# Kernel tuning notes

Measured on AMD Instinct MI355X. Metric: run time of the kernel, lower is better.

## Reference

```python
import jax, jax.numpy as jnp
import numpy as np

B, L, D, NH, K, R = 2, 1024, 768, 12, 24, 768
HD = D // NH            # head_dim = 64
NFFT = 2048             # nearest power of two >= 2*L-1


def _spectral_filters():
    # Hankel matrix Z_{ij} = 2 / ((i+j)^3 - (i+j)), top-K eigvecs scaled by sigma^{1/4}
    e = np.arange(1, L + 1, dtype=np.float64)
    ipj = e[:, None] + e[None, :]
    Z = 2.0 / (ipj ** 3 - ipj)
    sigma, phi = np.linalg.eigh(Z)
    phi_k = phi[:, -K:] * (sigma[-K:] ** 0.25)
    return jnp.asarray(phi_k, dtype=jnp.float32)  # (L, K)


def setup_inputs() -> dict:
    key = jax.random.key(0)
    ks = jax.random.split(key, 16)
    s = 0.02
    lin = lambda k_, i, o: jax.random.normal(k_, (i, o), jnp.float32) * s
    return {
        "x": jax.random.normal(ks[0], (B, L, D), jnp.float32),
        "stu_filters": _spectral_filters(),
        "M_inputs": jax.random.normal(ks[1], (D, R), jnp.float32) * s,
        "M_filters": jax.random.normal(ks[2], (K, R), jnp.float32) * s,
        "wq_w": lin(ks[3], D, D), "wq_b": jnp.zeros((D,), jnp.float32),
        "wk_w": lin(ks[4], D, D), "wk_b": jnp.zeros((D,), jnp.float32),
        "wv_w": lin(ks[5], D, D), "wv_b": jnp.zeros((D,), jnp.float32),
        "wg_w": lin(ks[6], D, D), "wg_b": jnp.zeros((D,), jnp.float32),
        "wo_w": lin(ks[7], D, D), "wo_b": jnp.zeros((D,), jnp.float32),
    }


def _stu_features(x, stu_filters, M_inputs, M_filters):
    # tensordot STU path: project inputs and filters to rank R, then FFT causal conv
    u = x @ M_inputs                       # (B, L, R)
    phi = stu_filters @ M_filters          # (L, R)
    sgn = jnp.where(jnp.arange(L) % 2 == 0, 1.0, -1.0)[None, :, None]  # (1, L, 1)
    V = jnp.fft.rfft(phi, n=NFFT, axis=0)  # (NFFT//2+1, R)
    U = jnp.stack([u, u * sgn], axis=-1)   # (B, L, R, 2)
    Uf = jnp.fft.rfft(U, n=NFFT, axis=1)   # (B, NFFT//2+1, R, 2)
    conv = jnp.fft.irfft(V[None, :, :, None] * Uf, n=NFFT, axis=1)[:, :L]  # (B, L, R, 2)
    u_plus = conv[..., 0]
    u_minus = conv[..., 1] * sgn
    return u_plus + u_minus               # (B, L, R) with R == D


def reference(x, stu_filters, M_inputs, M_filters,
              wq_w, wq_b, wk_w, wk_b, wv_w, wv_b,
              wg_w, wg_b, wo_w, wo_b):
    x_tilde = _stu_features(x, stu_filters, M_inputs, M_filters)  # (B, L, D)

    heads = lambda y: y.reshape(B, L, NH, HD).transpose(0, 2, 1, 3)  # (B, H, L, h)
    q = heads(x @ wq_w + wq_b)
    k = heads(x @ wk_w + wk_b)
    v = heads(x @ wv_w + wv_b)

    # causal linear attention via cumulative outer-product state
    Z = jnp.einsum('bhtp,bhtn->bhtpn', v, k)     # (B, H, L, h, h)
    Hc = jnp.cumsum(Z, axis=2)
    Y = jnp.einsum('bhtp,bhtpn->bhtn', q, Hc)    # (B, H, L, h)
    y_attn = Y.transpose(0, 2, 1, 3).reshape(B, L, D)

    gate = jax.nn.sigmoid(x @ wg_w + wg_b)
    y = x_tilde + (y_attn - x_tilde) * gate
    return y @ wo_w + wo_b
```

## Files before the change

kernel.cpp:

```cpp
#include <hip/hip_runtime.h>
#include <math.h>

#define B_  2
#define L_  1024
#define D_  768
#define NH_ 12
#define HD_ 64
#define K_  24
#define R_  768
#define NC_ 16
#define CS_ 64

typedef __bf16 bf16x8 __attribute__((ext_vector_type(8)));
typedef float f32x4 __attribute__((ext_vector_type(4)));
typedef float f32x8 __attribute__((ext_vector_type(8)));
typedef unsigned short u16x8 __attribute__((ext_vector_type(8)));

__device__ inline unsigned short f2bf(float f) {
    union { float f; unsigned u; } v; v.f = f;
    unsigned r = v.u + 0x7FFFu + ((v.u >> 16) & 1u);
    return (unsigned short)(r >> 16);
}

__device__ inline ushort4 pack4(const f32x4 v) {
    ushort4 r;
    r.x = f2bf(v[0]); r.y = f2bf(v[1]); r.z = f2bf(v[2]); r.w = f2bf(v[3]);
    return r;
}

__device__ inline u16x8 pack8(const f32x8 v) {
    u16x8 r;
#pragma unroll
    for (int e = 0; e < 8; ++e) r[e] = f2bf(v[e]);
    return r;
}

__device__ inline f32x8 bf2f8(const u16x8 v) {
    f32x8 r;
#pragma unroll
    for (int e = 0; e < 8; ++e) {
        union { float f; unsigned u; } t;
        t.u = ((unsigned)v[e]) << 16;
        r[e] = t.f;
    }
    return r;
}

#define GLD_LDS16(g, l)                                                     \
    __builtin_amdgcn_global_load_lds(                                       \
        (const __attribute__((address_space(1))) void*)(g),                 \
        (__attribute__((address_space(3))) void*)(l), 16, 0, 0)

__global__ __launch_bounds__(256) void k_prep(const float* __restrict__ w0,
                                              const float* __restrict__ w1,
                                              const float* __restrict__ w2,
                                              const float* __restrict__ w3,
                                              const float* __restrict__ w4,
                                              const float* __restrict__ w5,
                                              unsigned short* __restrict__ Wt,
                                              const float* __restrict__ x,
                                              unsigned short* __restrict__ xb) {
    const int bid = blockIdx.x;
    const int tid = threadIdx.x;
    if (bid < 864) {
        const int z = bid / 144, rem = bid % 144;
        const float* W;
        switch (z) {
            case 0: W = w0; break;
            case 1: W = w1; break;
            case 2: W = w2; break;
            case 3: W = w3; break;
            case 4: W = w4; break;
            default: W = w5; break;
        }
        unsigned short* o = Wt + (size_t)z * D_ * D_;
        __shared__ float t[64][69];
        const int n0 = (rem % 12) * 64, k0 = (rem / 12) * 64;
        const int row = tid >> 4, c4 = (tid & 15) * 4;
#pragma unroll
        for (int i = 0; i < 4; ++i) {
            const float4 v = *reinterpret_cast<const float4*>(
                W + (size_t)(k0 + row + i * 16) * D_ + n0 + c4);
            t[row + i * 16][c4 + 0] = v.x;
            t[row + i * 16][c4 + 1] = v.y;
            t[row + i * 16][c4 + 2] = v.z;
            t[row + i * 16][c4 + 3] = v.w;
        }
        __syncthreads();
        const int orow = tid >> 4, oc4 = (tid & 15) * 4;
#pragma unroll
        for (int i = 0; i < 4; ++i) {
            const int nn = orow + i * 16;
            ushort4 o4;
            o4.x = f2bf(t[oc4 + 0][nn]);
            o4.y = f2bf(t[oc4 + 1][nn]);
            o4.z = f2bf(t[oc4 + 2][nn]);
            o4.w = f2bf(t[oc4 + 3][nn]);
            *reinterpret_cast<ushort4*>(o + (size_t)(n0 + nn) * D_ + k0 + oc4) = o4;
        }
    } else {
        const int i8 = ((bid - 864) * 256 + tid) * 8;
        float4 f0 = *reinterpret_cast<const float4*>(x + i8);
        float4 f1 = *reinterpret_cast<const float4*>(x + i8 + 4);
        u16x8 p;
        p[0] = f2bf(f0.x); p[1] = f2bf(f0.y); p[2] = f2bf(f0.z); p[3] = f2bf(f0.w);
        p[4] = f2bf(f1.x); p[5] = f2bf(f1.y); p[6] = f2bf(f1.z); p[7] = f2bf(f1.w);
        *reinterpret_cast<u16x8*>(xb + i8) = p;
    }
}

template <int FM, int FN>
__device__ __forceinline__ void gemm_core(const unsigned short* __restrict__ A,
                                          const unsigned short* __restrict__ Bt,
                                          const float* __restrict__ bias,
                                          int mode,
                                          float* __restrict__ cf,
                                          unsigned short* __restrict__ cbf,
                                          unsigned short* __restrict__ ct,
                                          int N, int Kd,
                                          int bm, int bn, int tid) {
    constexpr int BM = 2 * FM * 16;
    constexpr int BN = 2 * FN * 16;
    constexpr int CTS = BM + 4;
    __shared__ unsigned short smem[2 * BM * 64 + 2 * BN * 64];
    unsigned short (*As)[BM * 64] = (unsigned short (*)[BM * 64])smem;
    unsigned short (*Bs)[BN * 64] = (unsigned short (*)[BN * 64])(smem + 2 * BM * 64);
    const int lane = tid & 63, wave = tid >> 6;
    const int wm = (wave >> 1) * (FM * 16), wn = (wave & 1) * (FN * 16);
    const int l15 = lane & 15, lg = lane >> 4;

    f32x4 acc[FM][FN] = {};

    auto stage = [&](int buf, int k0) {
#pragma unroll
        for (int q = 0; q < FM; ++q) {
            const int s = q * 256 + tid;
            GLD_LDS16(A + (size_t)(bm + (s >> 3)) * Kd + k0 + (s & 7) * 8,
                      &As[buf][s * 8]);
        }
#pragma unroll
        for (int q = 0; q < FN; ++q) {
            const int s = q * 256 + tid;
            GLD_LDS16(Bt + (size_t)(bn + (s >> 3)) * Kd + k0 + (s & 7) * 8,
                      &Bs[buf][s * 8]);
        }
    };

    stage(0, 0);
    __syncthreads();
    int cur = 0;
    const int nt = Kd / 64;
    for (int t = 0; t < nt; ++t) {
        if (t + 1 < nt) stage(cur ^ 1, (t + 1) * 64);
#pragma unroll
        for (int ks = 0; ks < 2; ++ks) {
            const int kb = ks * 32 + lg * 8;
            bf16x8 a[FM], b[FN];
#pragma unroll
            for (int f = 0; f < FM; ++f)
                a[f] = *reinterpret_cast<const bf16x8*>(
                    &As[cur][(wm + f * 16 + l15) * 64 + kb]);
#pragma unroll
            for (int f = 0; f < FN; ++f)
                b[f] = *reinterpret_cast<const bf16x8*>(
                    &Bs[cur][(wn + f * 16 + l15) * 64 + kb]);
#pragma unroll
            for (int fm = 0; fm < FM; ++fm)
#pragma unroll
                for (int fn = 0; fn < FN; ++fn)
                    acc[fm][fn] = __builtin_amdgcn_mfma_f32_16x16x32_bf16(
                        a[fm], b[fn], acc[fm][fn], 0, 0, 0);
        }
        __syncthreads();
        cur ^= 1;
    }

#pragma unroll
    for (int fm = 0; fm < FM; ++fm)
#pragma unroll
        for (int fn = 0; fn < FN; ++fn) {
            const int cl = wn + fn * 16 + l15;
            const int col = bn + cl;
            const float bv = bias ? bias[col] : 0.f;
            const int rl = wm + fm * 16 + lg * 4;
            const int r0 = bm + rl;
            f32x4 v = acc[fm][fn];
            v[0] += bv; v[1] += bv; v[2] += bv; v[3] += bv;
            if (mode == 0) {
#pragma unroll
                for (int j = 0; j < 4; ++j)
                    cf[(size_t)(r0 + j) * N + col] = v[j];
            }
            if (mode & 1) {
#pragma unroll
                for (int j = 0; j < 4; ++j)
                    cbf[(size_t)(r0 + j) * D_ + col] = f2bf(v[j]);
            }
            if (mode & 2) {
                *reinterpret_cast<ushort4*>(&smem[cl * CTS + rl]) = pack4(v);
            }
        }

    if (mode & 2) {
        __syncthreads();
        const int bI = bm >> 10, l0 = bm & 1023;
#pragma unroll
        for (int q = 0; q < BN * BM / 8 / 256; ++q) {
            const int slot = q * 256 + tid;
            const int cl = slot / (BM / 8), seg = slot % (BM / 8);
            const int gcol = bn + cl;
            const int h = gcol >> 6, n = gcol & 63;
            *reinterpret_cast<u16x8*>(
                ct + (((size_t)bI * NH_ + h) * 64 + n) * (size_t)L_ + l0 + seg * 8) =
                *reinterpret_cast<const u16x8*>(&smem[cl * CTS + seg * 8]);
        }
    }
}

__global__ __launch_bounds__(256) void k_gemm(const unsigned short* __restrict__ A,
                                              const unsigned short* __restrict__ Bt,
                                              const float* __restrict__ bias,
                                              float* __restrict__ C,
                                              int N, int Kd) {
    gemm_core<1, 2>(A, Bt, bias, 0, C, nullptr, nullptr, N, Kd,
                    blockIdx.y * 32, blockIdx.x * 64, threadIdx.x);
}

__global__ __launch_bounds__(256) void k_gemm5(const unsigned short* __restrict__ A,
                                               const unsigned short* __restrict__ wt,
                                               const float* __restrict__ bq,
                                               const float* __restrict__ bk,
                                               const float* __restrict__ bv,
                                               const float* __restrict__ bg,
                                               unsigned short* __restrict__ ubf,
                                               unsigned short* __restrict__ qbf,
                                               unsigned short* __restrict__ ktb,
                                               unsigned short* __restrict__ vbf,
                                               unsigned short* __restrict__ vtb,
                                               unsigned short* __restrict__ gbf) {
    const int z = blockIdx.z;
    const float* bias = nullptr;
    int mode = 1;
    unsigned short* cbf = nullptr; unsigned short* ct = nullptr;
    switch (z) {
        case 0: mode = 1; cbf = ubf; bias = nullptr; break;
        case 1: mode = 1; cbf = qbf; bias = bq; break;
        case 2: mode = 2; ct = ktb; bias = bk; break;
        case 3: mode = 3; cbf = vbf; ct = vtb; bias = bv; break;
        default: mode = 1; cbf = gbf; bias = bg; break;
    }
    const unsigned short* Bt = wt + (size_t)z * D_ * D_;
    gemm_core<4, 4>(A, Bt, bias, mode, nullptr, cbf, ct, D_, D_,
                    blockIdx.y * 128, blockIdx.x * 128, threadIdx.x);
}

__global__ __launch_bounds__(256) void k_attn(const unsigned short* __restrict__ qbf,
                                              const unsigned short* __restrict__ vbf,
                                              const unsigned short* __restrict__ ktb,
                                              const unsigned short* __restrict__ vtb,
                                              unsigned short* __restrict__ yab,
                                              const float* __restrict__ F,
                                              const float* __restrict__ Mf,
                                              unsigned short* __restrict__ phiev) {
    const int tid = threadIdx.x;
    if (blockIdx.x >= 384) {
        const int idx = ((int)blockIdx.x - 384) * 256 + tid;
        const int r = idx % R_;
        const int n = idx / R_;
        float acc = 0.f;
#pragma unroll
        for (int kk = 0; kk < K_; ++kk)
            acc += F[(2 * n) * K_ + kk] * Mf[kk * R_ + r];
        phiev[idx] = f2bf(2.f * acc);
        return;
    }
    const int c = blockIdx.x & 15, h = (blockIdx.x >> 4) % NH_, b = blockIdx.x / (16 * NH_);
    __shared__ unsigned short Qs[64 * 64];
    __shared__ unsigned short Vs[64 * 64];
    __shared__ unsigned short Kc[64 * 64];
    __shared__ unsigned short Tk[2][64 * 64];
    __shared__ unsigned short Tv[2][64 * 64];
    __shared__ unsigned short Sl[64 * 72];
    __shared__ unsigned short Hl[64 * 72];

    const int lane = tid & 63, wave = tid >> 6;
    const int wr = (wave >> 1) * 32, wc = (wave & 1) * 32;
    const int l15 = lane & 15, lg = lane >> 4;

    {
        const size_t rowbase = ((size_t)(b * L_ + c * CS_)) * D_ + h * HD_;
        const size_t tbase = ((size_t)(b * NH_ + h)) * 64 * (size_t)L_ + c * 64;
#pragma unroll
        for (int q2 = 0; q2 < 2; ++q2) {
            const int s = q2 * 256 + tid;
            const int row = s >> 3, c8 = s & 7;
            GLD_LDS16(qbf + rowbase + (size_t)row * D_ + c8 * 8, &Qs[s * 8]);
            GLD_LDS16(vbf + rowbase + (size_t)row * D_ + c8 * 8, &Vs[s * 8]);
            GLD_LDS16(ktb + tbase + (size_t)row * L_ + c8 * 8, &Kc[s * 8]);
        }
    }

    auto stage_t = [&](int buf, int cc) {
        const size_t tb2 = ((size_t)(b * NH_ + h)) * 64 * (size_t)L_ + cc * 64;
#pragma unroll
        for (int q2 = 0; q2 < 2; ++q2) {
            const int s = q2 * 256 + tid;
            const int row = s >> 3, c8 = s & 7;
            GLD_LDS16(ktb + tb2 + (size_t)row * L_ + c8 * 8, &Tk[buf][s * 8]);
            GLD_LDS16(vtb + tb2 + (size_t)row * L_ + c8 * 8, &Tv[buf][s * 8]);
        }
    };

    if (c > 0) stage_t(0, 0);
    __syncthreads();

    f32x4 hacc[2][2] = {};
    int cur = 0;
    for (int cc = 0; cc < c; ++cc) {
        if (cc + 1 < c) stage_t(cur ^ 1, cc + 1);
#pragma unroll
        for (int ks = 0; ks < 2; ++ks) {
            const int kb = ks * 32 + lg * 8;
            bf16x8 av[2], bk[2];
#pragma unroll
            for (int f = 0; f < 2; ++f) {
                av[f] = *reinterpret_cast<const bf16x8*>(&Tv[cur][(wr + f * 16 + l15) * 64 + kb]);
                bk[f] = *reinterpret_cast<const bf16x8*>(&Tk[cur][(wc + f * 16 + l15) * 64 + kb]);
            }
#pragma unroll
            for (int fm = 0; fm < 2; ++fm)
#pragma unroll
                for (int fn = 0; fn < 2; ++fn)
                    hacc[fm][fn] = __builtin_amdgcn_mfma_f32_16x16x32_bf16(
                        av[fm], bk[fn], hacc[fm][fn], 0, 0, 0);
        }
        __syncthreads();
        cur ^= 1;
    }

    if (c > 0) {
#pragma unroll
        for (int fm = 0; fm < 2; ++fm)
#pragma unroll
            for (int fn = 0; fn < 2; ++fn) {
                const int n = wc + fn * 16 + l15;
                const int p0 = wr + fm * 16 + lg * 4;
                *reinterpret_cast<ushort4*>(&Hl[n * 72 + p0]) = pack4(hacc[fm][fn]);
            }
    }

    {
        f32x4 sacc[2][2] = {};
#pragma unroll
        for (int ks = 0; ks < 2; ++ks) {
            const int kb = ks * 32 + lg * 8;
            bf16x8 av[2], bq[2];
#pragma unroll
            for (int f = 0; f < 2; ++f) {
                av[f] = *reinterpret_cast<const bf16x8*>(&Vs[(wr + f * 16 + l15) * 64 + kb]);
                bq[f] = *reinterpret_cast<const bf16x8*>(&Qs[(wc + f * 16 + l15) * 64 + kb]);
            }
#pragma unroll
            for (int fm = 0; fm < 2; ++fm)
#pragma unroll
                for (int fn = 0; fn < 2; ++fn)
                    sacc[fm][fn] = __builtin_amdgcn_mfma_f32_16x16x32_bf16(
                        av[fm], bq[fn], sacc[fm][fn], 0, 0, 0);
        }
#pragma unroll
        for (int fm = 0; fm < 2; ++fm)
#pragma unroll
            for (int fn = 0; fn < 2; ++fn) {
                const int t = wc + fn * 16 + l15;
                const int s0 = wr + fm * 16 + lg * 4;
#pragma unroll
                for (int j = 0; j < 4; ++j)
                    if (s0 + j > t) sacc[fm][fn][j] = 0.f;
                *reinterpret_cast<ushort4*>(&Sl[t * 72 + s0]) = pack4(sacc[fm][fn]);
            }
    }
    __syncthreads();

    f32x4 yacc[2][2] = {};
#pragma unroll
    for (int ks = 0; ks < 2; ++ks) {
        const int kb = ks * 32 + lg * 8;
        bf16x8 ak[2], bs[2];
#pragma unroll
        for (int f = 0; f < 2; ++f) {
            ak[f] = *reinterpret_cast<const bf16x8*>(&Kc[(wr + f * 16 + l15) * 64 + kb]);
            bs[f] = *reinterpret_cast<const bf16x8*>(&Sl[(wc + f * 16 + l15) * 72 + kb]);
        }
#pragma unroll
        for (int fm = 0; fm < 2; ++fm)
#pragma unroll
            for (int fn = 0; fn < 2; ++fn)
                yacc[fm][fn] = __builtin_amdgcn_mfma_f32_16x16x32_bf16(
                    ak[fm], bs[fn], yacc[fm][fn], 0, 0, 0);
    }
    if (c > 0) {
#pragma unroll
        for (int ks = 0; ks < 2; ++ks) {
            const int kb = ks * 32 + lg * 8;
            bf16x8 ah[2], bq[2];
#pragma unroll
            for (int f = 0; f < 2; ++f) {
                ah[f] = *reinterpret_cast<const bf16x8*>(&Hl[(wr + f * 16 + l15) * 72 + kb]);
                bq[f] = *reinterpret_cast<const bf16x8*>(&Qs[(wc + f * 16 + l15) * 64 + kb]);
            }
#pragma unroll
            for (int fm = 0; fm < 2; ++fm)
#pragma unroll
                for (int fn = 0; fn < 2; ++fn)
                    yacc[fm][fn] = __builtin_amdgcn_mfma_f32_16x16x32_bf16(
                        ah[fm], bq[fn], yacc[fm][fn], 0, 0, 0);
        }
    }

#pragma unroll
    for (int fm = 0; fm < 2; ++fm)
#pragma unroll
        for (int fn = 0; fn < 2; ++fn) {
            const int n0 = wr + fm * 16 + lg * 4;
            const int t = wc + fn * 16 + l15;
            const size_t idx = ((size_t)(b * L_ + c * CS_ + t)) * D_ + h * HD_ + n0;
            *reinterpret_cast<ushort4*>(yab + idx) = pack4(yacc[fm][fn]);
        }
}

__global__ __launch_bounds__(768) void k_conv(const unsigned short* __restrict__ ubf,
                                              const unsigned short* __restrict__ phiev,
                                              const unsigned short* __restrict__ yab,
                                              const unsigned short* __restrict__ gbf,
                                              unsigned short* __restrict__ gx) {
    __shared__ u16x8 red[8][8][96];
    const int tid = threadIdx.x;
    const int g   = tid / 96;
    const int lr  = tid % 96;
    const int r   = lr * 8;
    const int m0  = blockIdx.x * 8;
    const int bp  = blockIdx.y;
    const int b   = bp >> 1, p = bp & 1;

    f32x8 acc[8] = {};
    f32x8 w[8]   = {};

    const int ns = g * 64;
    const int ne = min(ns + 64, m0 + 8);

    if (ns < ne) {
        if (g > 0) {
#pragma unroll
            for (int j = 1; j <= 7; ++j)
                w[(8 - j) & 7] = bf2f8(
                    *reinterpret_cast<const u16x8*>(phiev + (size_t)(ns - j) * R_ + r));
        }
        const unsigned short* pp = phiev + (size_t)ns * R_ + r;
        const unsigned short* up =
            ubf + ((size_t)(b * L_) + (size_t)(2 * (m0 + 7 - ns) + p)) * R_ + r;
        for (int i = ns; i < ne; i += 8) {
#pragma unroll
            for (int k = 0; k < 8; ++k) {
                const u16x8 pv = *reinterpret_cast<const u16x8*>(pp);
                const u16x8 uv = *reinterpret_cast<const u16x8*>(up);
                w[k] = bf2f8(pv);
                const f32x8 fu = bf2f8(uv);
#pragma unroll
                for (int a = 0; a < 8; ++a)
                    acc[a] += w[(k + a + 1) & 7] * fu;
                pp += R_;
                up -= 2 * R_;
            }
        }
    }

#pragma unroll
    for (int a = 0; a < 8; ++a) red[g][a][lr] = pack8(acc[a]);
    __syncthreads();

    const int a2 = tid / 96, l2 = tid % 96;
    f32x8 s = {};
#pragma unroll
    for (int g2 = 0; g2 < 8; ++g2) s += bf2f8(red[g2][a2][l2]);

    const size_t idx = ((size_t)(b * L_) + (size_t)(2 * (m0 + a2) + p)) * R_ + l2 * 8;
    const f32x8 yf = bf2f8(*reinterpret_cast<const u16x8*>(yab + idx));
    const f32x8 gf = bf2f8(*reinterpret_cast<const u16x8*>(gbf + idx));
    u16x8 o;
#pragma unroll
    for (int e = 0; e < 8; ++e) {
        const float sg = 1.f / (1.f + expf(-gf[e]));
        o[e] = f2bf(s[e] + (yf[e] - s[e]) * sg);
    }
    *reinterpret_cast<u16x8*>(gx + idx) = o;
}

extern "C" void kernel_launch(void* const* d_in, const int* in_sizes, int n_in,
                              void* d_out, int out_size, void* d_ws, size_t ws_size,
                              hipStream_t stream) {
    const float* x    = (const float*)d_in[0];
    const float* stu  = (const float*)d_in[1];
    const float* Mi   = (const float*)d_in[2];
    const float* Mf   = (const float*)d_in[3];
    const float* wq_w = (const float*)d_in[4];
    const float* wq_b = (const float*)d_in[5];
    const float* wk_w = (const float*)d_in[6];
    const float* wk_b = (const float*)d_in[7];
    const float* wv_w = (const float*)d_in[8];
    const float* wv_b = (const float*)d_in[9];
    const float* wg_w = (const float*)d_in[10];
    const float* wg_b = (const float*)d_in[11];
    const float* wo_w = (const float*)d_in[12];
    const float* wo_b = (const float*)d_in[13];
    float* out = (float*)d_out;

    char* ws = (char*)d_ws;
    size_t o = 0;
    const size_t WSZ = (size_t)D_ * D_;
    unsigned short* wbf   = (unsigned short*)(ws + o); o += 6 * WSZ * 2;
    unsigned short* xbf   = (unsigned short*)(ws + o); o += (size_t)B_ * L_ * D_ * 2;
    unsigned short* gx    = (unsigned short*)(ws + o); o += (size_t)B_ * L_ * D_ * 2;
    unsigned short* qbf   = (unsigned short*)(ws + o); o += (size_t)B_ * L_ * D_ * 2;
    unsigned short* vbf   = (unsigned short*)(ws + o); o += (size_t)B_ * L_ * D_ * 2;
    unsigned short* ubf   = (unsigned short*)(ws + o); o += (size_t)B_ * L_ * D_ * 2;
    unsigned short* gbf   = (unsigned short*)(ws + o); o += (size_t)B_ * L_ * D_ * 2;
    unsigned short* yab   = (unsigned short*)(ws + o); o += (size_t)B_ * L_ * D_ * 2;
    unsigned short* ktb   = (unsigned short*)(ws + o); o += (size_t)B_ * NH_ * 64 * L_ * 2;
    unsigned short* vtb   = (unsigned short*)(ws + o); o += (size_t)B_ * NH_ * 64 * L_ * 2;
    unsigned short* phiev = (unsigned short*)(ws + o); o += (size_t)(L_ / 2) * R_ * 2;

    unsigned short* wo_t = wbf + 5 * WSZ;

    const dim3 blk(256);

    k_prep<<<dim3(1632), blk, 0, stream>>>(Mi, wq_w, wk_w, wv_w, wg_w, wo_w, wbf,
                                           x, xbf);

    k_gemm5<<<dim3(D_ / 128, (B_ * L_) / 128, 5), blk, 0, stream>>>(
        xbf, wbf, wq_b, wk_b, wv_b, wg_b, ubf, qbf, ktb, vbf, vtb, gbf);

    k_attn<<<dim3(384 + 1536), blk, 0, stream>>>(qbf, vbf, ktb, vtb, yab,
                                                 stu, Mf, phiev);

    k_conv<<<dim3(L_ / 2 / 8, B_ * 2), dim3(768), 0, stream>>>(ubf, phiev, yab, gbf, gx);

    k_gemm<<<dim3(D_ / 64, (B_ * L_) / 32), blk, 0, stream>>>(gx, wo_t, wo_b, out, D_, D_);
}
```

Measured before the change: 91.94 us.

## Merge conv into attention kernel, fuse gating into output GEMM, move phi prep

The phi filter projection moves into the prep kernel. The STU causal convolution now runs as extra blocks of the attention kernel, using 2 partition groups of 256 instead of 8 of 64. The sigmoid gating blend moves into the A-tile staging of the output GEMM, which drops one kernel launch and the gx intermediate round trip. The cost is heavier sequential work per conv thread with fewer parallel groups, and gate math recomputed for each N-tile of the output GEMM.

```diff
diff --git a/kernel.cpp b/kernel.cpp
--- a/kernel.cpp
+++ b/kernel.cpp
@@ -59,7 +59,10 @@
                                               const float* __restrict__ w5,
                                               unsigned short* __restrict__ Wt,
                                               const float* __restrict__ x,
-                                              unsigned short* __restrict__ xb) {
+                                              unsigned short* __restrict__ xb,
+                                              const float* __restrict__ F,
+                                              const float* __restrict__ Mf,
+                                              unsigned short* __restrict__ phiev) {
     const int bid = blockIdx.x;
     const int tid = threadIdx.x;
     if (bid < 864) {
@@ -87,18 +90,17 @@
             t[row + i * 16][c4 + 3] = v.w;
         }
         __syncthreads();
-        const int orow = tid >> 4, oc4 = (tid & 15) * 4;
 #pragma unroll
         for (int i = 0; i < 4; ++i) {
-            const int nn = orow + i * 16;
+            const int nn = row + i * 16;
             ushort4 o4;
-            o4.x = f2bf(t[oc4 + 0][nn]);
-            o4.y = f2bf(t[oc4 + 1][nn]);
-            o4.z = f2bf(t[oc4 + 2][nn]);
-            o4.w = f2bf(t[oc4 + 3][nn]);
-            *reinterpret_cast<ushort4*>(o + (size_t)(n0 + nn) * D_ + k0 + oc4) = o4;
-        }
-    } else {
+            o4.x = f2bf(t[c4 + 0][nn]);
+            o4.y = f2bf(t[c4 + 1][nn]);
+            o4.z = f2bf(t[c4 + 2][nn]);
+            o4.w = f2bf(t[c4 + 3][nn]);
+            *reinterpret_cast<ushort4*>(o + (size_t)(n0 + nn) * D_ + k0 + c4) = o4;
+        }
+    } else if (bid < 1632) {
         const int i8 = ((bid - 864) * 256 + tid) * 8;
         float4 f0 = *reinterpret_cast<const float4*>(x + i8);
         float4 f1 = *reinterpret_cast<const float4*>(x + i8 + 4);
@@ -106,6 +108,15 @@
         p[0] = f2bf(f0.x); p[1] = f2bf(f0.y); p[2] = f2bf(f0.z); p[3] = f2bf(f0.w);
         p[4] = f2bf(f1.x); p[5] = f2bf(f1.y); p[6] = f2bf(f1.z); p[7] = f2bf(f1.w);
         *reinterpret_cast<u16x8*>(xb + i8) = p;
+    } else {
+        const int idx = (bid - 1632) * 256 + tid;
+        const int r = idx % R_;
+        const int n = idx / R_;
+        float acc = 0.f;
+#pragma unroll
+        for (int kk = 0; kk < K_; ++kk)
+            acc += F[(2 * n) * K_ + kk] * Mf[kk * R_ + r];
+        phiev[idx] = f2bf(2.f * acc);
     }
 }
 
@@ -114,17 +125,17 @@
                                           const unsigned short* __restrict__ Bt,
                                           const float* __restrict__ bias,
                                           int mode,
-                                          float* __restrict__ cf,
                                           unsigned short* __restrict__ cbf,
                                           unsigned short* __restrict__ ct,
-                                          int N, int Kd,
-                                          int bm, int bn, int tid) {
+                                          int Kd, int bm, int bn, int tid) {
     constexpr int BM = 2 * FM * 16;
     constexpr int BN = 2 * FN * 16;
     constexpr int CTS = BM + 4;
-    __shared__ unsigned short smem[2 * BM * 64 + 2 * BN * 64];
-    unsigned short (*As)[BM * 64] = (unsigned short (*)[BM * 64])smem;
-    unsigned short (*Bs)[BN * 64] = (unsigned short (*)[BN * 64])(smem + 2 * BM * 64);
+    __shared__ __align__(16) unsigned short sm[2 * BM * 64 + 2 * BN * 64];
+    unsigned short* As0 = sm;
+    unsigned short* As1 = sm + BM * 64;
+    unsigned short* Bs0 = sm + 2 * BM * 64;
+    unsigned short* Bs1 = sm + 2 * BM * 64 + BN * 64;
     const int lane = tid & 63, wave = tid >> 6;
     const int wm = (wave >> 1) * (FM * 16), wn = (wave & 1) * (FN * 16);
     const int l15 = lane & 15, lg = lane >> 4;
@@ -132,17 +143,19 @@
     f32x4 acc[FM][FN] = {};
 
     auto stage = [&](int buf, int k0) {
+        unsigned short* as = buf ? As1 : As0;
+        unsigned short* bs = buf ? Bs1 : Bs0;
 #pragma unroll
         for (int q = 0; q < FM; ++q) {
             const int s = q * 256 + tid;
             GLD_LDS16(A + (size_t)(bm + (s >> 3)) * Kd + k0 + (s & 7) * 8,
-                      &As[buf][s * 8]);
+                      &as[s * 8]);
         }
 #pragma unroll
         for (int q = 0; q < FN; ++q) {
             const int s = q * 256 + tid;
             GLD_LDS16(Bt + (size_t)(bn + (s >> 3)) * Kd + k0 + (s & 7) * 8,
-                      &Bs[buf][s * 8]);
+                      &bs[s * 8]);
         }
     };
 
@@ -152,18 +165,18 @@
     const int nt = Kd / 64;
     for (int t = 0; t < nt; ++t) {
         if (t + 1 < nt) stage(cur ^ 1, (t + 1) * 64);
+        const unsigned short* as = cur ? As1 : As0;
+        const unsigned short* bs = cur ? Bs1 : Bs0;
 #pragma unroll
         for (int ks = 0; ks < 2; ++ks) {
             const int kb = ks * 32 + lg * 8;
             bf16x8 a[FM], b[FN];
 #pragma unroll
             for (int f = 0; f < FM; ++f)
-                a[f] = *reinterpret_cast<const bf16x8*>(
-                    &As[cur][(wm + f * 16 + l15) * 64 + kb]);
+                a[f] = *reinterpret_cast<const bf16x8*>(&as[(wm + f * 16 + l15) * 64 + kb]);
 #pragma unroll
             for (int f = 0; f < FN; ++f)
-                b[f] = *reinterpret_cast<const bf16x8*>(
-                    &Bs[cur][(wn + f * 16 + l15) * 64 + kb]);
+                b[f] = *reinterpret_cast<const bf16x8*>(&bs[(wn + f * 16 + l15) * 64 + kb]);
 #pragma unroll
             for (int fm = 0; fm < FM; ++fm)
 #pragma unroll
@@ -186,18 +199,13 @@
             const int r0 = bm + rl;
             f32x4 v = acc[fm][fn];
             v[0] += bv; v[1] += bv; v[2] += bv; v[3] += bv;
-            if (mode == 0) {
-#pragma unroll
-                for (int j = 0; j < 4; ++j)
-                    cf[(size_t)(r0 + j) * N + col] = v[j];
-            }
             if (mode & 1) {
 #pragma unroll
                 for (int j = 0; j < 4; ++j)
                     cbf[(size_t)(r0 + j) * D_ + col] = f2bf(v[j]);
             }
             if (mode & 2) {
-                *reinterpret_cast<ushort4*>(&smem[cl * CTS + rl]) = pack4(v);
+                *reinterpret_cast<ushort4*>(&sm[cl * CTS + rl]) = pack4(v);
             }
         }
 
@@ -212,18 +220,9 @@
             const int h = gcol >> 6, n = gcol & 63;
             *reinterpret_cast<u16x8*>(
                 ct + (((size_t)bI * NH_ + h) * 64 + n) * (size_t)L_ + l0 + seg * 8) =
-                *reinterpret_cast<const u16x8*>(&smem[cl * CTS + seg * 8]);
-        }
-    }
-}
-
-__global__ __launch_bounds__(256) void k_gemm(const unsigned short* __restrict__ A,
-                                              const unsigned short* __restrict__ Bt,
-                                              const float* __restrict__ bias,
-                                              float* __restrict__ C,
-                                              int N, int Kd) {
-    gemm_core<1, 2>(A, Bt, bias, 0, C, nullptr, nullptr, N, Kd,
-                    blockIdx.y * 32, blockIdx.x * 64, threadIdx.x);
+                *reinterpret_cast<const u16x8*>(&sm[cl * CTS + seg * 8]);
+        }
+    }
 }
 
 __global__ __launch_bounds__(256) void k_gemm5(const unsigned short* __restrict__ A,
@@ -249,39 +248,89 @@
         case 3: mode = 3; cbf = vbf; ct = vtb; bias = bv; break;
         default: mode = 1; cbf = gbf; bias = bg; break;
     }
-    const unsigned short* Bt = wt + (size_t)z * D_ * D_;
-    gemm_core<4, 4>(A, Bt, bias, mode, nullptr, cbf, ct, D_, D_,
-                    blockIdx.y * 128, blockIdx.x * 128, threadIdx.x);
-}
-
-__global__ __launch_bounds__(256) void k_attn(const unsigned short* __restrict__ qbf,
-                                              const unsigned short* __restrict__ vbf,
-                                              const unsigned short* __restrict__ ktb,
-                                              const unsigned short* __restrict__ vtb,
-                                              unsigned short* __restrict__ yab,
-                                              const float* __restrict__ F,
-                                              const float* __restrict__ Mf,
-                                              unsigned short* __restrict__ phiev) {
+    gemm_core<4, 4>(A, wt + (size_t)z * D_ * D_, bias, mode, cbf, ct,
+                    D_, blockIdx.y * 128, blockIdx.x * 128, threadIdx.x);
+}
+
+__global__ __launch_bounds__(256) void k_attnconv(const unsigned short* __restrict__ qbf,
+                                                  const unsigned short* __restrict__ vbf,
+                                                  const unsigned short* __restrict__ ktb,
+                                                  const unsigned short* __restrict__ vtb,
+                                                  unsigned short* __restrict__ yab,
+                                                  const unsigned short* __restrict__ ubf,
+                                                  const unsigned short* __restrict__ phiev,
+                                                  unsigned short* __restrict__ xtb) {
+    __shared__ __align__(16) char smem_raw[75776];
+    unsigned short* sm16 = (unsigned short*)smem_raw;
     const int tid = threadIdx.x;
+
     if (blockIdx.x >= 384) {
-        const int idx = ((int)blockIdx.x - 384) * 256 + tid;
-        const int r = idx % R_;
-        const int n = idx / R_;
-        float acc = 0.f;
-#pragma unroll
-        for (int kk = 0; kk < K_; ++kk)
-            acc += F[(2 * n) * K_ + kk] * Mf[kk * R_ + r];
-        phiev[idx] = f2bf(2.f * acc);
+        const int cu = (int)blockIdx.x - 384;
+        const int m0 = (cu & 63) * 8;
+        const int bp = cu >> 6;
+        const int b = bp >> 1, p = bp & 1;
+        u16x8* red = (u16x8*)sm16;
+
+        if (tid < 192) {
+            const int g = tid / 96, lr = tid % 96;
+            const int r = lr * 8;
+            f32x8 acc[8] = {};
+            f32x8 w[8] = {};
+            const int ns = g * 256;
+            const int ne = min(ns + 256, m0 + 8);
+            if (ns < ne) {
+                if (g > 0) {
+#pragma unroll
+                    for (int j = 1; j <= 7; ++j)
+                        w[(8 - j) & 7] = bf2f8(*reinterpret_cast<const u16x8*>(
+                            phiev + (size_t)(ns - j) * R_ + r));
+                }
+                const unsigned short* pp = phiev + (size_t)ns * R_ + r;
+                const unsigned short* up =
+                    ubf + ((size_t)(b * L_) + (size_t)(2 * (m0 + 7 - ns) + p)) * R_ + r;
+                for (int i = ns; i < ne; i += 8) {
+#pragma unroll
+                    for (int k = 0; k < 8; ++k) {
+                        const u16x8 pv = *reinterpret_cast<const u16x8*>(pp);
+                        const u16x8 uv = *reinterpret_cast<const u16x8*>(up);
+                        w[k] = bf2f8(pv);
+                        const f32x8 fu = bf2f8(uv);
+#pragma unroll
+                        for (int a = 0; a < 8; ++a)
+                            acc[a] += w[(k + a + 1) & 7] * fu;
+                        pp += R_;
+                        up -= 2 * R_;
+                    }
+                }
+            }
+#pragma unroll
+            for (int a = 0; a < 8; ++a) red[(g * 8 + a) * 96 + lr] = pack8(acc[a]);
+        }
+        __syncthreads();
+
+#pragma unroll
+        for (int q = 0; q < 3; ++q) {
+            const int slot = q * 256 + tid;
+            const int a2 = slot / 96, l2 = slot % 96;
+            f32x8 s = bf2f8(red[(0 * 8 + a2) * 96 + l2]) +
+                      bf2f8(red[(1 * 8 + a2) * 96 + l2]);
+            const size_t idx =
+                ((size_t)(b * L_) + (size_t)(2 * (m0 + a2) + p)) * R_ + l2 * 8;
+            *reinterpret_cast<u16x8*>(xtb + idx) = pack8(s);
+        }
         return;
     }
+
     const int c = blockIdx.x & 15, h = (blockIdx.x >> 4) % NH_, b = blockIdx.x / (16 * NH_);
-    __shared__ unsigned short Qs[64 * 64];
-    __shared__ unsigned short Vs[64 * 64];
-    __shared__ unsigned short Kc[64 * 64];
-    __shared__ unsigned short Tk[2][64 * 64];
-    __shared__ unsigned short Tv[2][64 * 64];
-    __shared__ unsigned short Sl[64 * 72];
-    __shared__ unsigned short Hl[64 * 72];
+    unsigned short* Qs  = sm16;
+    unsigned short* Vs  = sm16 + 4096;
+    unsigned short* Kc  = sm16 + 8192;
+    unsigned short* Tk0 = sm16 + 12288;
+    unsigned short* Tk1 = sm16 + 16384;
+    unsigned short* Tv0 = sm16 + 20480;
+    unsigned short* Tv1 = sm16 + 24576;
+    unsigned short* Sl  = sm16 + 28672;
+    unsigned short* Hl  = sm16 + 33280;
 
     const int lane = tid & 63, wave = tid >> 6;
     const int wr = (wave >> 1) * 32, wc = (wave & 1) * 32;
@@ -301,13 +350,15 @@
     }
 
     auto stage_t = [&](int buf, int cc) {
+        unsigned short* tk = buf ? Tk1 : Tk0;
+        unsigned short* tv = buf ? Tv1 : Tv0;
         const size_t tb2 = ((size_t)(b * NH_ + h)) * 64 * (size_t)L_ + cc * 64;
 #pragma unroll
         for (int q2 = 0; q2 < 2; ++q2) {
             const int s = q2 * 256 + tid;
             const int row = s >> 3, c8 = s & 7;
-            GLD_LDS16(ktb + tb2 + (size_t)row * L_ + c8 * 8, &Tk[buf][s * 8]);
-            GLD_LDS16(vtb + tb2 + (size_t)row * L_ + c8 * 8, &Tv[buf][s * 8]);
+            GLD_LDS16(ktb + tb2 + (size_t)row * L_ + c8 * 8, &tk[s * 8]);
+            GLD_LDS16(vtb + tb2 + (size_t)row * L_ + c8 * 8, &tv[s * 8]);
         }
     };
 
@@ -318,14 +369,16 @@
     int cur = 0;
     for (int cc = 0; cc < c; ++cc) {
         if (cc + 1 < c) stage_t(cur ^ 1, cc + 1);
+        const unsigned short* tk = cur ? Tk1 : Tk0;
+        const unsigned short* tv = cur ? Tv1 : Tv0;
 #pragma unroll
         for (int ks = 0; ks < 2; ++ks) {
             const int kb = ks * 32 + lg * 8;
             bf16x8 av[2], bk[2];
 #pragma unroll
             for (int f = 0; f < 2; ++f) {
-                av[f] = *reinterpret_cast<const bf16x8*>(&Tv[cur][(wr + f * 16 + l15) * 64 + kb]);
-                bk[f] = *reinterpret_cast<const bf16x8*>(&Tk[cur][(wc + f * 16 + l15) * 64 + kb]);
+                av[f] = *reinterpret_cast<const bf16x8*>(&tv[(wr + f * 16 + l15) * 64 + kb]);
+                bk[f] = *reinterpret_cast<const bf16x8*>(&tk[(wc + f * 16 + l15) * 64 + kb]);
             }
 #pragma unroll
             for (int fm = 0; fm < 2; ++fm)
@@ -428,71 +481,83 @@
         }
 }
 
-__global__ __launch_bounds__(768) void k_conv(const unsigned short* __restrict__ ubf,
-                                              const unsigned short* __restrict__ phiev,
-                                              const unsigned short* __restrict__ yab,
-                                              const unsigned short* __restrict__ gbf,
-                                              unsigned short* __restrict__ gx) {
-    __shared__ u16x8 red[8][8][96];
+__global__ __launch_bounds__(256) void k_outgemm(const unsigned short* __restrict__ xtb,
+                                                 const unsigned short* __restrict__ yab,
+                                                 const unsigned short* __restrict__ gbf,
+                                                 const unsigned short* __restrict__ Bt,
+                                                 const float* __restrict__ bias,
+                                                 float* __restrict__ C) {
+    constexpr int BM = 32, BN = 64;
+    __shared__ __align__(16) unsigned short sm[2 * BM * 64 + 2 * BN * 64];
+    unsigned short* As0 = sm;
+    unsigned short* As1 = sm + BM * 64;
+    unsigned short* Bs0 = sm + 2 * BM * 64;
+    unsigned short* Bs1 = sm + 2 * BM * 64 + BN * 64;
     const int tid = threadIdx.x;
-    const int g   = tid / 96;
-    const int lr  = tid % 96;
-    const int r   = lr * 8;
-    const int m0  = blockIdx.x * 8;
-    const int bp  = blockIdx.y;
-    const int b   = bp >> 1, p = bp & 1;
-
-    f32x8 acc[8] = {};
-    f32x8 w[8]   = {};
-
-    const int ns = g * 64;
-    const int ne = min(ns + 64, m0 + 8);
-
-    if (ns < ne) {
-        if (g > 0) {
-#pragma unroll
-            for (int j = 1; j <= 7; ++j)
-                w[(8 - j) & 7] = bf2f8(
-                    *reinterpret_cast<const u16x8*>(phiev + (size_t)(ns - j) * R_ + r));
-        }
-        const unsigned short* pp = phiev + (size_t)ns * R_ + r;
-        const unsigned short* up =
-            ubf + ((size_t)(b * L_) + (size_t)(2 * (m0 + 7 - ns) + p)) * R_ + r;
-        for (int i = ns; i < ne; i += 8) {
-#pragma unroll
-            for (int k = 0; k < 8; ++k) {
-                const u16x8 pv = *reinterpret_cast<const u16x8*>(pp);
-                const u16x8 uv = *reinterpret_cast<const u16x8*>(up);
-                w[k] = bf2f8(pv);
-                const f32x8 fu = bf2f8(uv);
-#pragma unroll
-                for (int a = 0; a < 8; ++a)
-                    acc[a] += w[(k + a + 1) & 7] * fu;
-                pp += R_;
-                up -= 2 * R_;
-            }
-        }
-    }
-
-#pragma unroll
-    for (int a = 0; a < 8; ++a) red[g][a][lr] = pack8(acc[a]);
+    const int bm = blockIdx.y * BM, bn = blockIdx.x * BN;
+    const int lane = tid & 63, wave = tid >> 6;
+    const int wm = (wave >> 1) * 16, wn = (wave & 1) * 32;
+    const int l15 = lane & 15, lg = lane >> 4;
+
+    f32x4 acc[1][2] = {};
+
+    auto stage = [&](int buf, int k0) {
+        {
+            unsigned short* as = buf ? As1 : As0;
+            const int row = tid >> 3, c8 = tid & 7;
+            const size_t idx = (size_t)(bm + row) * D_ + k0 + c8 * 8;
+            const f32x8 xv = bf2f8(*reinterpret_cast<const u16x8*>(xtb + idx));
+            const f32x8 yv = bf2f8(*reinterpret_cast<const u16x8*>(yab + idx));
+            const f32x8 gv = bf2f8(*reinterpret_cast<const u16x8*>(gbf + idx));
+            f32x8 o;
+#pragma unroll
+            for (int e = 0; e < 8; ++e) {
+                const float sg = 1.f / (1.f + expf(-gv[e]));
+                o[e] = xv[e] + (yv[e] - xv[e]) * sg;
+            }
+            *reinterpret_cast<u16x8*>(&as[tid * 8]) = pack8(o);
+        }
+        {
+            unsigned short* bs = buf ? Bs1 : Bs0;
+#pragma unroll
+            for (int q = 0; q < 2; ++q) {
+                const int s = q * 256 + tid;
+                GLD_LDS16(Bt + (size_t)(bn + (s >> 3)) * D_ + k0 + (s & 7) * 8,
+                          &bs[s * 8]);
+            }
+        }
+    };
+
+    stage(0, 0);
     __syncthreads();
-
-    const int a2 = tid / 96, l2 = tid % 96;
-    f32x8 s = {};
-#pragma unroll
-    for (int g2 = 0; g2 < 8; ++g2) s += bf2f8(red[g2][a2][l2]);
-
-    const size_t idx = ((size_t)(b * L_) + (size_t)(2 * (m0 + a2) + p)) * R_ + l2 * 8;
-    const f32x8 yf = bf2f8(*reinterpret_cast<const u16x8*>(yab + idx));
-    const f32x8 gf = bf2f8(*reinterpret_cast<const u16x8*>(gbf + idx));
-    u16x8 o;
-#pragma unroll
-    for (int e = 0; e < 8; ++e) {
-        const float sg = 1.f / (1.f + expf(-gf[e]));
-        o[e] = f2bf(s[e] + (yf[e] - s[e]) * sg);
-    }
-    *reinterpret_cast<u16x8*>(gx + idx) = o;
+    int cur = 0;
+    const int nt = D_ / 64;
+    for (int t = 0; t < nt; ++t) {
+        if (t + 1 < nt) stage(cur ^ 1, (t + 1) * 64);
+        const unsigned short* as = cur ? As1 : As0;
+        const unsigned short* bs = cur ? Bs1 : Bs0;
+#pragma unroll
+        for (int ks = 0; ks < 2; ++ks) {
+            const int kb = ks * 32 + lg * 8;
+            bf16x8 a0 = *reinterpret_cast<const bf16x8*>(&as[(wm + l15) * 64 + kb]);
+            bf16x8 b0 = *reinterpret_cast<const bf16x8*>(&bs[(wn + l15) * 64 + kb]);
+            bf16x8 b1 = *reinterpret_cast<const bf16x8*>(&bs[(wn + 16 + l15) * 64 + kb]);
+            acc[0][0] = __builtin_amdgcn_mfma_f32_16x16x32_bf16(a0, b0, acc[0][0], 0, 0, 0);
+            acc[0][1] = __builtin_amdgcn_mfma_f32_16x16x32_bf16(a0, b1, acc[0][1], 0, 0, 0);
+        }
+        __syncthreads();
+        cur ^= 1;
+    }
+
+#pragma unroll
+    for (int fn = 0; fn < 2; ++fn) {
+        const int col = bn + wn + fn * 16 + l15;
+        const float bv = bias[col];
+        const int r0 = bm + wm + lg * 4;
+#pragma unroll
+        for (int j = 0; j < 4; ++j)
+            C[(size_t)(r0 + j) * D_ + col] = acc[0][fn][j] + bv;
+    }
 }
 
 extern "C" void kernel_launch(void* const* d_in, const int* in_sizes, int n_in,
@@ -519,12 +584,12 @@
     const size_t WSZ = (size_t)D_ * D_;
     unsigned short* wbf   = (unsigned short*)(ws + o); o += 6 * WSZ * 2;
     unsigned short* xbf   = (unsigned short*)(ws + o); o += (size_t)B_ * L_ * D_ * 2;
-    unsigned short* gx    = (unsigned short*)(ws + o); o += (size_t)B_ * L_ * D_ * 2;
     unsigned short* qbf   = (unsigned short*)(ws + o); o += (size_t)B_ * L_ * D_ * 2;
     unsigned short* vbf   = (unsigned short*)(ws + o); o += (size_t)B_ * L_ * D_ * 2;
     unsigned short* ubf   = (unsigned short*)(ws + o); o += (size_t)B_ * L_ * D_ * 2;
     unsigned short* gbf   = (unsigned short*)(ws + o); o += (size_t)B_ * L_ * D_ * 2;
     unsigned short* yab   = (unsigned short*)(ws + o); o += (size_t)B_ * L_ * D_ * 2;
+    unsigned short* xtb   = (unsigned short*)(ws + o); o += (size_t)B_ * L_ * D_ * 2;
     unsigned short* ktb   = (unsigned short*)(ws + o); o += (size_t)B_ * NH_ * 64 * L_ * 2;
     unsigned short* vtb   = (unsigned short*)(ws + o); o += (size_t)B_ * NH_ * 64 * L_ * 2;
     unsigned short* phiev = (unsigned short*)(ws + o); o += (size_t)(L_ / 2) * R_ * 2;
@@ -533,16 +598,15 @@
 
     const dim3 blk(256);
 
-    k_prep<<<dim3(1632), blk, 0, stream>>>(Mi, wq_w, wk_w, wv_w, wg_w, wo_w, wbf,
-                                           x, xbf);
+    k_prep<<<dim3(3168), blk, 0, stream>>>(Mi, wq_w, wk_w, wv_w, wg_w, wo_w, wbf,
+                                           x, xbf, stu, Mf, phiev);
 
     k_gemm5<<<dim3(D_ / 128, (B_ * L_) / 128, 5), blk, 0, stream>>>(
         xbf, wbf, wq_b, wk_b, wv_b, wg_b, ubf, qbf, ktb, vbf, vtb, gbf);
 
-    k_attn<<<dim3(384 + 1536), blk, 0, stream>>>(qbf, vbf, ktb, vtb, yab,
-                                                 stu, Mf, phiev);
-
-    k_conv<<<dim3(L_ / 2 / 8, B_ * 2), dim3(768), 0, stream>>>(ubf, phiev, yab, gbf, gx);
-
-    k_gemm<<<dim3(D_ / 64, (B_ * L_) / 32), blk, 0, stream>>>(gx, wo_t, wo_b, out, D_, D_);
-}
+    k_attnconv<<<dim3(640), blk, 0, stream>>>(qbf, vbf, ktb, vtb, yab,
+                                              ubf, phiev, xtb);
+
+    k_outgemm<<<dim3(D_ / 64, (B_ * L_) / 32), blk, 0, stream>>>(
+        xtb, yab, gbf, wo_t, wo_b, out);
+}
```

New measurement: 117.3 us. 1.28x slower.
